# Optimization experiments

Measured on AMD Instinct MI355X. Metric: run time of the kernel, lower is better.

The kernel has to match this reference:

```python
import jax, jax.numpy as jnp
import numpy as np

B, P, D_IN, D_MOD, N_HEADS = 512, 64, 64, 256, 4

def _ln(x, g, b):
    m = x.mean(-1, keepdims=True)
    v = ((x - m) ** 2).mean(-1, keepdims=True)
    return (x - m) / jnp.sqrt(v + 1e-5) * g + b

def _lin(x, w, b):
    return x @ w.T + b

def _mha(q, k, v, in_w, in_b, out_w, out_b, n_heads):
    # Faithful to torch nn.MultiheadAttention(batch_first=False): dim0=seq, dim1=batch.
    S, N, E = q.shape
    dh = E // n_heads
    wq, wk, wv = jnp.split(in_w, 3, axis=0)
    bq, bk, bv = jnp.split(in_b, 3)
    qp = _lin(q, wq, bq).reshape(S, N, n_heads, dh)
    kp = _lin(k, wk, bk).reshape(S, N, n_heads, dh)
    vp = _lin(v, wv, bv).reshape(S, N, n_heads, dh)
    scores = jnp.einsum('snhd,tnhd->nhst', qp, kp) * (1.0 / np.sqrt(dh))
    attn = jax.nn.softmax(scores, axis=-1)
    o = jnp.einsum('nhst,tnhd->snhd', attn, vp).reshape(S, N, E)
    return _lin(o, out_w, out_b)

def _forward(x, emb_w, emb_b, emb_g, emb_beta, post_w, post_b, post_g, post_beta,
             attn_qw, attn_qb, attn_kw, attn_kb, attn_vw, attn_vb,
             attn_inw, attn_inb, attn_outw, attn_outb, attn_g, attn_beta,
             player_w, player_b, player_g, player_beta,
             team_w, team_b, team_g, team_beta,
             pre_w, pre_b, pre_g, pre_beta, lnf_g, lnf_b, pred_w, pred_b):
    # embedding: LinearWithLayerNorm = LayerNorm(Linear(x))
    p = _ln(_lin(x, emb_w, emb_b), emb_g, emb_beta)
    # post_embedding: ResidualLinearWithLayerNorm = LayerNorm(Linear(x)) + x
    p = _ln(_lin(p, post_w, post_b), post_g, post_beta) + p
    for i in range(2):
        res = p
        q = _lin(p, attn_qw[i], attn_qb[i])
        k = _lin(p, attn_kw[i], attn_kb[i])
        v = _lin(p, attn_vw[i], attn_vb[i])
        a = _mha(q, k, v, attn_inw[i], attn_inb[i], attn_outw[i], attn_outb[i], N_HEADS)
        p = _ln(a, attn_g[i], attn_beta[i]) + res
    for i in range(2):
        p = _ln(_lin(p, player_w[i], player_b[i]), player_g[i], player_beta[i]) + p
    # segment reduce: padded-ragged scatter + sum == masked sum over the player axis.
    # NOTE: original code computes BOTH masks as original[:,:,-1]==1 (bug preserved).
    mask = (x[:, :, -1] == 1).astype(p.dtype)  # [B, P]
    home = jnp.einsum('bpd,bp->bd', p, mask)
    away = home
    teams = jnp.concatenate([home, away], axis=1)  # [B, 2*d_mod]
    for i in range(2):
        teams = _ln(_lin(teams, team_w[i], team_b[i]), team_g[i], team_beta[i]) + teams
    o = _ln(_lin(teams, pre_w, pre_b), pre_g, pre_beta)
    o = _ln(o, lnf_g, lnf_b)
    o = _lin(o, pred_w, pred_b)[:, 0]  # squeeze(dim=1)
    return o


def setup_inputs() -> dict:
    key = jax.random.key(0)
    ks = iter(jax.random.split(key, 64))
    def nrm(shape):
        return jax.random.normal(next(ks), shape, jnp.float32) * 0.02
    x = jax.random.normal(next(ks), (B, P, D_IN), jnp.float32)
    flag = jax.random.bernoulli(next(ks), 0.5, (B, P)).astype(jnp.float32)
    x = x.at[:, :, -1].set(flag)  # binary home-team indicator channel
    d, d2 = D_MOD, 2 * D_MOD
    return dict(
        x=x,
        emb_w=nrm((d, D_IN)), emb_b=jnp.zeros(d), emb_g=jnp.ones(d), emb_beta=jnp.zeros(d),
        post_w=nrm((d, d)), post_b=jnp.zeros(d), post_g=jnp.ones(d), post_beta=jnp.zeros(d),
        attn_qw=nrm((2, d, d)), attn_qb=jnp.zeros((2, d)),
        attn_kw=nrm((2, d, d)), attn_kb=jnp.zeros((2, d)),
        attn_vw=nrm((2, d, d)), attn_vb=jnp.zeros((2, d)),
        attn_inw=nrm((2, 3 * d, d)), attn_inb=jnp.zeros((2, 3 * d)),
        attn_outw=nrm((2, d, d)), attn_outb=jnp.zeros((2, d)),
        attn_g=jnp.ones((2, d)), attn_beta=jnp.zeros((2, d)),
        player_w=nrm((2, d, d)), player_b=jnp.zeros((2, d)),
        player_g=jnp.ones((2, d)), player_beta=jnp.zeros((2, d)),
        team_w=nrm((2, d2, d2)), team_b=jnp.zeros((2, d2)),
        team_g=jnp.ones((2, d2)), team_beta=jnp.zeros((2, d2)),
        pre_w=nrm((d, d2)), pre_b=jnp.zeros(d), pre_g=jnp.ones(d), pre_beta=jnp.zeros(d),
        lnf_g=jnp.ones(d), lnf_b=jnp.zeros(d),
        pred_w=nrm((1, d)), pred_b=jnp.zeros(1),
    )


def reference(x, emb_w, emb_b, emb_g, emb_beta, post_w, post_b, post_g, post_beta,
              attn_qw, attn_qb, attn_kw, attn_kb, attn_vw, attn_vb,
              attn_inw, attn_inb, attn_outw, attn_outb, attn_g, attn_beta,
              player_w, player_b, player_g, player_beta,
              team_w, team_b, team_g, team_beta,
              pre_w, pre_b, pre_g, pre_beta, lnf_g, lnf_b, pred_w, pred_b):
    return _forward(x, emb_w, emb_b, emb_g, emb_beta, post_w, post_b, post_g, post_beta,
                    attn_qw, attn_qb, attn_kw, attn_kb, attn_vw, attn_vb,
                    attn_inw, attn_inb, attn_outw, attn_outb, attn_g, attn_beta,
                    player_w, player_b, player_g, player_beta,
                    team_w, team_b, team_g, team_beta,
                    pre_w, pre_b, pre_g, pre_beta, lnf_g, lnf_b, pred_w, pred_b)
```

## Files before the change

kernel.cpp:

```cpp
#include <hip/hip_runtime.h>
#include <math.h>


typedef __bf16 bf16x8 __attribute__((ext_vector_type(8)));
typedef __bf16 bf16x4 __attribute__((ext_vector_type(4)));
typedef __bf16 bf16x2 __attribute__((ext_vector_type(2)));
typedef float  f32x4  __attribute__((ext_vector_type(4)));
typedef unsigned short u16;
typedef unsigned short u16x8 __attribute__((ext_vector_type(8)));

__device__ __forceinline__ u16 f2b(float f) {
    unsigned int u = __builtin_bit_cast(unsigned int, f);
    return (u16)((u + 0x7fffu + ((u >> 16) & 1u)) >> 16);
}
__device__ __forceinline__ float b2f(u16 u) {
    unsigned int v = ((unsigned int)u) << 16;
    return __builtin_bit_cast(float, v);
}
__device__ __forceinline__ bf16x8 ld2x64(const u16* p) {
    bf16x4 lo = *(const bf16x4*)p;
    bf16x4 hi = *(const bf16x4*)(p + 4);
    return __builtin_shufflevector(lo, hi, 0, 1, 2, 3, 4, 5, 6, 7);
}
__device__ __forceinline__ bf16x8 ld4x32(const u16* p) {
    bf16x2 a = *(const bf16x2*)p,     b = *(const bf16x2*)(p + 2);
    bf16x2 c = *(const bf16x2*)(p + 4), d = *(const bf16x2*)(p + 6);
    bf16x4 lo = __builtin_shufflevector(a, b, 0, 1, 2, 3);
    bf16x4 hi = __builtin_shufflevector(c, d, 0, 1, 2, 3);
    return __builtin_shufflevector(lo, hi, 0, 1, 2, 3, 4, 5, 6, 7);
}
__device__ __forceinline__ void split8(const float* __restrict__ s,
                                       bf16x8& hi, bf16x8& lo) {
    u16x8 h, l;
    #pragma unroll
    for (int j = 0; j < 8; ++j) {
        float v  = s[j];
        u16  hb  = f2b(v);
        h[j] = hb;
        l[j] = f2b(v - b2f(hb));
    }
    hi = __builtin_bit_cast(bf16x8, h);
    lo = __builtin_bit_cast(bf16x8, l);
}

template<int IN, bool LN, bool RES, bool AF32, int OMODE>
__device__ __forceinline__
void gemm_body(const void* __restrict__ Xa, const void* __restrict__ Xb, int ldX,
               const u16* __restrict__ Whi, const u16* __restrict__ Wlo,
               const float* __restrict__ bias,
               const float* __restrict__ g, const float* __restrict__ beta,
               const u16* __restrict__ resh, const u16* __restrict__ resl,
               int ldRes, void* __restrict__ Y0, void* __restrict__ Y1, int ldY,
               u16* __restrict__ Wb)
{
    constexpr int KT = IN / 32;
    const int tid = threadIdx.x;
    const int wv = tid >> 6, lane = tid & 63;
    const int quad = lane >> 4, l16 = lane & 15;
    const long arow = (long)blockIdx.x * 64 + wv * 16 + l16;

    const u16* sbase[8];
    int sdst[8];
    #pragma unroll
    for (int i = 0; i < 8; ++i) {
        int cid = tid + i * 256;
        int plane = cid >> 10, nt = (cid >> 6) & 15, slot = cid & 63;
        int q = slot >> 4, c = slot & 15;
        sbase[i] = (plane ? Wlo : Whi) + (long)(nt * 16 + c) * IN + q * 8;
        sdst[i]  = (plane * 16 + nt) * 512 + slot * 8;
    }
    u16x8 wreg[8];
    auto issueW = [&](int kt) {
        #pragma unroll
        for (int i = 0; i < 8; ++i) wreg[i] = *(const u16x8*)(sbase[i] + kt * 32);
    };
    auto commitW = [&](int buf) {
        #pragma unroll
        for (int i = 0; i < 8; ++i)
            *(u16x8*)&Wb[buf * 16384 + sdst[i]] = wreg[i];
    };

    bf16x8 ah[3], al[3];
    auto loadA = [&](int kt) {
        int s = kt % 3;
        long aofs = arow * (long)ldX + kt * 32 + quad * 8;
        if constexpr (AF32) {
            float av[8];
            *(f32x4*)&av[0] = *(const f32x4*)&((const float*)Xa)[aofs];
            *(f32x4*)&av[4] = *(const f32x4*)&((const float*)Xa)[aofs + 4];
            split8(av, ah[s], al[s]);
        } else {
            ah[s] = *(const bf16x8*)&((const u16*)Xa)[aofs];
            al[s] = *(const bf16x8*)&((const u16*)Xb)[aofs];
        }
    };

    f32x4 acc[16];
    #pragma unroll
    for (int nt = 0; nt < 16; ++nt) acc[nt] = f32x4{0.f, 0.f, 0.f, 0.f};

    issueW(0);
    commitW(0);
    if (KT > 1) issueW(1);
    loadA(0);
    if (KT > 1) loadA(1);
    __syncthreads();

    #pragma unroll
    for (int kt = 0; kt < KT; ++kt) {
        if (kt + 2 < KT) loadA(kt + 2);
        const u16* wb = Wb + (kt & 1) * 16384;
        const int s = kt % 3;
        #pragma unroll
        for (int nt = 0; nt < 16; ++nt) {
            bf16x8 bhi = *(const bf16x8*)&wb[nt * 512 + lane * 8];
            bf16x8 blo = *(const bf16x8*)&wb[(16 + nt) * 512 + lane * 8];
            acc[nt] = __builtin_amdgcn_mfma_f32_16x16x32_bf16(al[s], bhi, acc[nt], 0, 0, 0);
            acc[nt] = __builtin_amdgcn_mfma_f32_16x16x32_bf16(ah[s], blo, acc[nt], 0, 0, 0);
            acc[nt] = __builtin_amdgcn_mfma_f32_16x16x32_bf16(ah[s], bhi, acc[nt], 0, 0, 0);
        }
        if (kt + 1 < KT) {
            commitW((kt + 1) & 1);
            if (kt + 2 < KT) issueW(kt + 2);
            __syncthreads();
        }
    }

    #pragma unroll
    for (int nt = 0; nt < 16; ++nt) {
        float bc = bias[nt * 16 + l16];
        #pragma unroll
        for (int r = 0; r < 4; ++r) acc[nt][r] += bc;
    }

    float mean[4], rstd[4];
    if constexpr (LN) {
        float s1[4] = {0, 0, 0, 0}, s2[4] = {0, 0, 0, 0};
        #pragma unroll
        for (int nt = 0; nt < 16; ++nt)
            #pragma unroll
            for (int r = 0; r < 4; ++r) {
                s1[r] += acc[nt][r];
                s2[r] += acc[nt][r] * acc[nt][r];
            }
        #pragma unroll
        for (int off = 1; off < 16; off <<= 1)
            #pragma unroll
            for (int r = 0; r < 4; ++r) {
                s1[r] += __shfl_xor(s1[r], off, 64);
                s2[r] += __shfl_xor(s2[r], off, 64);
            }
        #pragma unroll
        for (int r = 0; r < 4; ++r) {
            mean[r] = s1[r] * (1.0f / 256.f);
            float var = s2[r] * (1.0f / 256.f) - mean[r] * mean[r];
            rstd[r] = rsqrtf(var + 1e-5f);
        }
    }
    #pragma unroll
    for (int nt = 0; nt < 16; ++nt) {
        int col = nt * 16 + l16;
        float gc = 1.f, bc2 = 0.f;
        if constexpr (LN) { gc = g[col]; bc2 = beta[col]; }
        #pragma unroll
        for (int r = 0; r < 4; ++r) {
            long row = (long)blockIdx.x * 64 + wv * 16 + quad * 4 + r;
            float v = acc[nt][r];
            if constexpr (LN) v = (v - mean[r]) * rstd[r] * gc + bc2;
            if constexpr (RES)
                v += b2f(resh[row * ldRes + col]) + b2f(resl[row * ldRes + col]);
            long yofs = row * ldY + col;
            if constexpr (OMODE == 0) {
                ((float*)Y0)[yofs] = v;
            } else if constexpr (OMODE == 1) {
                u16 hb = f2b(v);
                ((u16*)Y0)[yofs] = hb;
                ((u16*)Y1)[yofs] = f2b(v - b2f(hb));
            } else {
                ((u16*)Y0)[yofs] = f2b(v);
            }
        }
    }
}

template<int IN, bool LN, bool RES, bool AF32, int OMODE>
__global__ __launch_bounds__(256)
void gemm_kernel(const void* __restrict__ Xa, const void* __restrict__ Xb, int ldX,
                 const u16* __restrict__ Whi, const u16* __restrict__ Wlo,
                 const float* __restrict__ bias,
                 const float* __restrict__ g, const float* __restrict__ beta,
                 const u16* __restrict__ resh, const u16* __restrict__ resl,
                 int ldRes, void* __restrict__ Y0, void* __restrict__ Y1, int ldY)
{
    __shared__ u16 Wb[32768];
    gemm_body<IN, LN, RES, AF32, OMODE>(Xa, Xb, ldX, Whi, Wlo, bias, g,
                                        beta, resh, resl, ldRes, Y0, Y1,
                                        ldY, Wb);
}

__global__ __launch_bounds__(256)
void qkv_proj(const u16* __restrict__ ph, const u16* __restrict__ pl,
              const u16* __restrict__ cwL, const float* __restrict__ cb,
              u16* __restrict__ qb, u16* __restrict__ kb, u16* __restrict__ vh)
{
    __shared__ u16 Wb[32768];
    int wsel = blockIdx.y;
    const u16* whi = cwL + (long)wsel * 65536;
    const u16* wlo = cwL + 393216 + (long)wsel * 65536;
    u16* Y = (wsel == 0) ? qb : (wsel == 1) ? kb : vh;
    gemm_body<256, false, false, false, 2>(
        ph, pl, 256, whi, wlo, cb + wsel * 256, nullptr, nullptr,
        nullptr, nullptr, 0, Y, nullptr, 256, Wb);
}

__global__ __launch_bounds__(256)
void combine_kernel(const float* __restrict__ inw, const float* __restrict__ inb,
                    const float* __restrict__ qw, const float* __restrict__ kw,
                    const float* __restrict__ vw, const float* __restrict__ qb,
                    const float* __restrict__ kb, const float* __restrict__ vb,
                    u16* __restrict__ cw, float* __restrict__ cb)
{
    int idx = blockIdx.y, L = idx / 3, wsel = idx % 3;
    const float* Wa = inw + (long)L * 768 * 256 + wsel * 65536;
    const float* ba = inb + L * 768 + wsel * 256;
    const float* Wf = (wsel == 0 ? qw : wsel == 1 ? kw : vw) + (long)L * 65536;
    const float* bf = (wsel == 0 ? qb : wsel == 1 ? kb : vb) + L * 256;

    int o = blockIdx.x, j = threadIdx.x;
    float s = 0.f;
    for (int mm = 0; mm < 256; ++mm)
        s += Wa[o * 256 + mm] * Wf[mm * 256 + j];
    u16 hb = f2b(s);
    cw[(long)idx * 65536 + o * 256 + j] = hb;
    cw[393216 + (long)idx * 65536 + o * 256 + j] = f2b(s - b2f(hb));

    __shared__ float red[256];
    red[j] = Wa[o * 256 + j] * bf[j];
    __syncthreads();
    for (int st = 128; st > 0; st >>= 1) {
        if (j < st) red[j] += red[j + st];
        __syncthreads();
    }
    if (j == 0) cb[idx * 256 + o] = red[0] + ba[o];
}

__global__ __launch_bounds__(256)
void cast_split_multi(const float* s0, u16* d0, int n0,
                      const float* s1, u16* d1, int n1,
                      const float* s2, u16* d2, int n2,
                      const float* s3, u16* d3, int n3,
                      const float* s4, u16* d4, int n4,
                      const float* s5, u16* d5, int n5)
{
    const float* s; u16* d; int n;
    switch (blockIdx.y) {
        case 0: s = s0; d = d0; n = n0; break;
        case 1: s = s1; d = d1; n = n1; break;
        case 2: s = s2; d = d2; n = n2; break;
        case 3: s = s3; d = d3; n = n3; break;
        case 4: s = s4; d = d4; n = n4; break;
        default: s = s5; d = d5; n = n5; break;
    }
    int i = (blockIdx.x * 256 + threadIdx.x) * 4;
    if (i >= n) return;
    float4 v = *(const float4*)&s[i];
    ushort4 h, l;
    h.x = f2b(v.x); l.x = f2b(v.x - b2f(h.x));
    h.y = f2b(v.y); l.y = f2b(v.y - b2f(h.y));
    h.z = f2b(v.z); l.z = f2b(v.z - b2f(h.z));
    h.w = f2b(v.w); l.w = f2b(v.w - b2f(h.w));
    *(ushort4*)&d[i] = h;
    *(ushort4*)&d[n + i] = l;
}

#define VTS 66
#define PS  68
#define EXP2SCALE 0.18033688089184986f

__global__ __launch_bounds__(256)
void attn_kernel(const u16* __restrict__ qbuf, const u16* __restrict__ kbuf,
                 const u16* __restrict__ vh,
                 u16* __restrict__ ofh, u16* __restrict__ ofl)
{
    const int n = blockIdx.x, h = blockIdx.y, sq = blockIdx.z;
    const int tid = threadIdx.x;
    const int wv = tid >> 6, lane = tid & 63;
    const int quad = lane >> 4, l16 = lane & 15;

    __shared__ u16 Vth[64 * VTS];
    __shared__ u16 Pbh[4][32 * PS];

    bf16x8 qf[2][2];
    #pragma unroll
    for (int rt = 0; rt < 2; ++rt)
        #pragma unroll
        for (int kc = 0; kc < 2; ++kc) {
            long s = sq * 128 + wv * 32 + rt * 16 + l16;
            qf[rt][kc] = *(const bf16x8*)&qbuf[(s * 64 + n) * 256 + h * 64
                                               + kc * 32 + quad * 8];
        }

    f32x4 o[2][4];
    #pragma unroll
    for (int rt = 0; rt < 2; ++rt)
        #pragma unroll
        for (int dt = 0; dt < 4; ++dt) o[rt][dt] = f32x4{0.f, 0.f, 0.f, 0.f};
    float l_run[2][4] = {{0.f, 0.f, 0.f, 0.f}, {0.f, 0.f, 0.f, 0.f}};

    for (int tb = 0; tb < 8; ++tb) {
        __syncthreads();
        for (int i = tid; i < 512; i += 256) {
            int t = i >> 3, c = i & 7;
            u16x8 hvv = *(const u16x8*)&vh[((long)(tb * 64 + t) * 64 + n) * 256
                                           + h * 64 + c * 8];
            #pragma unroll
            for (int j = 0; j < 8; ++j)
                Vth[(c * 8 + j) * VTS + t] = hvv[j];
        }
        __syncthreads();

        f32x4 sA[2][4];
        #pragma unroll
        for (int rt = 0; rt < 2; ++rt)
            #pragma unroll
            for (int tt = 0; tt < 4; ++tt) sA[rt][tt] = f32x4{0.f, 0.f, 0.f, 0.f};
        #pragma unroll
        for (int kc = 0; kc < 2; ++kc)
            #pragma unroll
            for (int tt = 0; tt < 4; ++tt) {
                bf16x8 kf = *(const bf16x8*)
                    &kbuf[((long)(tb * 64 + tt * 16 + l16) * 64 + n) * 256
                          + h * 64 + kc * 32 + quad * 8];
                sA[0][tt] = __builtin_amdgcn_mfma_f32_16x16x32_bf16(
                    qf[0][kc], kf, sA[0][tt], 0, 0, 0);
                sA[1][tt] = __builtin_amdgcn_mfma_f32_16x16x32_bf16(
                    qf[1][kc], kf, sA[1][tt], 0, 0, 0);
            }

        #pragma unroll
        for (int rt = 0; rt < 2; ++rt)
            #pragma unroll
            for (int r = 0; r < 4; ++r) {
                float p0 = exp2f(sA[rt][0][r] * EXP2SCALE);
                float p1 = exp2f(sA[rt][1][r] * EXP2SCALE);
                float p2 = exp2f(sA[rt][2][r] * EXP2SCALE);
                float p3 = exp2f(sA[rt][3][r] * EXP2SCALE);
                int prow = (rt * 16 + quad * 4 + r) * PS + l16;
                Pbh[wv][prow +  0] = f2b(p0);
                Pbh[wv][prow + 16] = f2b(p1);
                Pbh[wv][prow + 32] = f2b(p2);
                Pbh[wv][prow + 48] = f2b(p3);
                l_run[rt][r] += (p0 + p1) + (p2 + p3);
            }

        #pragma unroll
        for (int kc = 0; kc < 2; ++kc) {
            bf16x8 pfh[2];
            #pragma unroll
            for (int rt = 0; rt < 2; ++rt)
                pfh[rt] = ld2x64(&Pbh[wv][(rt * 16 + l16) * PS
                                          + kc * 32 + quad * 8]);
            #pragma unroll
            for (int dt = 0; dt < 4; ++dt) {
                bf16x8 vfh = ld4x32(&Vth[(dt * 16 + l16) * VTS
                                         + kc * 32 + quad * 8]);
                o[0][dt] = __builtin_amdgcn_mfma_f32_16x16x32_bf16(
                    pfh[0], vfh, o[0][dt], 0, 0, 0);
                o[1][dt] = __builtin_amdgcn_mfma_f32_16x16x32_bf16(
                    pfh[1], vfh, o[1][dt], 0, 0, 0);
            }
        }
    }

    #pragma unroll
    for (int off = 1; off < 16; off <<= 1)
        #pragma unroll
        for (int rt = 0; rt < 2; ++rt)
            #pragma unroll
            for (int r = 0; r < 4; ++r)
                l_run[rt][r] += __shfl_xor(l_run[rt][r], off, 64);

    #pragma unroll
    for (int rt = 0; rt < 2; ++rt)
        #pragma unroll
        for (int r = 0; r < 4; ++r) {
            float inv = 1.0f / l_run[rt][r];
            long s = sq * 128 + wv * 32 + rt * 16 + quad * 4 + r;
            #pragma unroll
            for (int dt = 0; dt < 4; ++dt) {
                long idx = (s * 64 + n) * 256 + h * 64 + dt * 16 + l16;
                float val = o[rt][dt][r] * inv;
                u16 hb = f2b(val);
                ofh[idx] = hb;
                ofl[idx] = f2b(val - b2f(hb));
            }
        }
}

__global__ __launch_bounds__(256)
void team_reduce_kernel(const float* __restrict__ x, const u16* __restrict__ ph,
                        const u16* __restrict__ pl, float* __restrict__ teams)
{
    int b = blockIdx.x, d = threadIdx.x;
    float acc = 0.f;
    for (int pp = 0; pp < 64; ++pp) {
        float flag = x[((long)b * 64 + pp) * 64 + 63];
        if (flag == 1.0f) {
            long idx = ((long)b * 64 + pp) * 256 + d;
            acc += b2f(ph[idx]) + b2f(pl[idx]);
        }
    }
    teams[(long)b * 512 + d]       = acc;
    teams[(long)b * 512 + 256 + d] = acc;
}

template<int IN, int OUT, bool RES>
__global__ __launch_bounds__(256)
void tail_gemm(const float* __restrict__ X,
               const u16* __restrict__ Whi, const u16* __restrict__ Wlo,
               const float* __restrict__ bias,
               const float* __restrict__ g, const float* __restrict__ beta,
               const float* __restrict__ res, float* __restrict__ Y)
{
    constexpr int NTW = OUT / 64;
    constexpr int KT  = IN / 32;
    const int tid = threadIdx.x;
    const int wv = tid >> 6, lane = tid & 63;
    const int quad = lane >> 4, l16 = lane & 15;
    const int row0 = blockIdx.x * 16;
    const int colbase = wv * (OUT / 4);

    f32x4 acc[NTW];
    #pragma unroll
    for (int nt = 0; nt < NTW; ++nt) acc[nt] = f32x4{0.f, 0.f, 0.f, 0.f};

    #pragma unroll
    for (int kt = 0; kt < KT; ++kt) {
        float av[8];
        long aofs = (long)(row0 + l16) * IN + kt * 32 + quad * 8;
        *(f32x4*)&av[0] = *(const f32x4*)&X[aofs];
        *(f32x4*)&av[4] = *(const f32x4*)&X[aofs + 4];
        bf16x8 ah, al;
        split8(av, ah, al);
        #pragma unroll
        for (int nt = 0; nt < NTW; ++nt) {
            long wofs = (long)(colbase + nt * 16 + l16) * IN + kt * 32 + quad * 8;
            bf16x8 bhi = *(const bf16x8*)&Whi[wofs];
            bf16x8 blo = *(const bf16x8*)&Wlo[wofs];
            acc[nt] = __builtin_amdgcn_mfma_f32_16x16x32_bf16(al, bhi, acc[nt], 0, 0, 0);
            acc[nt] = __builtin_amdgcn_mfma_f32_16x16x32_bf16(ah, blo, acc[nt], 0, 0, 0);
            acc[nt] = __builtin_amdgcn_mfma_f32_16x16x32_bf16(ah, bhi, acc[nt], 0, 0, 0);
        }
    }

    #pragma unroll
    for (int nt = 0; nt < NTW; ++nt) {
        float bc = bias[colbase + nt * 16 + l16];
        #pragma unroll
        for (int r = 0; r < 4; ++r) acc[nt][r] += bc;
    }

    float s1[4] = {0, 0, 0, 0}, s2[4] = {0, 0, 0, 0};
    #pragma unroll
    for (int nt = 0; nt < NTW; ++nt)
        #pragma unroll
        for (int r = 0; r < 4; ++r) {
            s1[r] += acc[nt][r];
            s2[r] += acc[nt][r] * acc[nt][r];
        }
    #pragma unroll
    for (int off = 1; off < 16; off <<= 1)
        #pragma unroll
        for (int r = 0; r < 4; ++r) {
            s1[r] += __shfl_xor(s1[r], off, 64);
            s2[r] += __shfl_xor(s2[r], off, 64);
        }
    __shared__ float r1[64], r2[64];
    if (l16 == 0) {
        #pragma unroll
        for (int r = 0; r < 4; ++r) {
            r1[wv * 16 + quad * 4 + r] = s1[r];
            r2[wv * 16 + quad * 4 + r] = s2[r];
        }
    }
    __syncthreads();
    float mean[4], rstd[4];
    #pragma unroll
    for (int r = 0; r < 4; ++r) {
        int rr = quad * 4 + r;
        float t1 = r1[rr] + r1[16 + rr] + r1[32 + rr] + r1[48 + rr];
        float t2 = r2[rr] + r2[16 + rr] + r2[32 + rr] + r2[48 + rr];
        mean[r] = t1 * (1.0f / OUT);
        float var = t2 * (1.0f / OUT) - mean[r] * mean[r];
        rstd[r] = rsqrtf(var + 1e-5f);
    }
    #pragma unroll
    for (int nt = 0; nt < NTW; ++nt) {
        int col = colbase + nt * 16 + l16;
        float gc = g[col], bc2 = beta[col];
        #pragma unroll
        for (int r = 0; r < 4; ++r) {
            int row = row0 + quad * 4 + r;
            float v = (acc[nt][r] - mean[r]) * rstd[r] * gc + bc2;
            if constexpr (RES) v += res[(long)row * OUT + col];
            Y[(long)row * OUT + col] = v;
        }
    }
}

__global__ __launch_bounds__(64)
void ln_kernel(const float* __restrict__ X, const float* __restrict__ g,
               const float* __restrict__ b, float* __restrict__ Y)
{
    int row = blockIdx.x, lane = threadIdx.x;
    float4 v = *(const float4*)&X[(long)row * 256 + lane * 4];
    float s1 = v.x + v.y + v.z + v.w;
    float s2 = v.x*v.x + v.y*v.y + v.z*v.z + v.w*v.w;
    #pragma unroll
    for (int off = 32; off > 0; off >>= 1) {
        s1 += __shfl_xor(s1, off, 64);
        s2 += __shfl_xor(s2, off, 64);
    }
    float mean = s1 * (1.f / 256.f);
    float rstd = rsqrtf(s2 * (1.f / 256.f) - mean * mean + 1e-5f);
    float4 gg = *(const float4*)&g[lane * 4];
    float4 bb = *(const float4*)&b[lane * 4];
    float4 o;
    o.x = (v.x - mean) * rstd * gg.x + bb.x;
    o.y = (v.y - mean) * rstd * gg.y + bb.y;
    o.z = (v.z - mean) * rstd * gg.z + bb.z;
    o.w = (v.w - mean) * rstd * gg.w + bb.w;
    *(float4*)&Y[(long)row * 256 + lane * 4] = o;
}

__global__ __launch_bounds__(64)
void pred_kernel(const float* __restrict__ X, const float* __restrict__ pw,
                 const float* __restrict__ pb, float* __restrict__ out)
{
    int row = blockIdx.x, lane = threadIdx.x;
    float4 v = *(const float4*)&X[(long)row * 256 + lane * 4];
    float4 w = *(const float4*)&pw[lane * 4];
    float s = v.x*w.x + v.y*w.y + v.z*w.z + v.w*w.w;
    #pragma unroll
    for (int off = 32; off > 0; off >>= 1) s += __shfl_xor(s, off, 64);
    if (lane == 0) out[row] = s + pb[0];
}

extern "C" void kernel_launch(void* const* d_in, const int* in_sizes, int n_in,
                              void* d_out, int out_size, void* d_ws, size_t ws_size,
                              hipStream_t stream)
{
    const float* x         = (const float*)d_in[0];
    const float* emb_w     = (const float*)d_in[1];
    const float* emb_b     = (const float*)d_in[2];
    const float* emb_g     = (const float*)d_in[3];
    const float* emb_beta  = (const float*)d_in[4];
    const float* post_w    = (const float*)d_in[5];
    const float* post_b    = (const float*)d_in[6];
    const float* post_g    = (const float*)d_in[7];
    const float* post_beta = (const float*)d_in[8];
    const float* attn_qw   = (const float*)d_in[9];
    const float* attn_qb   = (const float*)d_in[10];
    const float* attn_kw   = (const float*)d_in[11];
    const float* attn_kb   = (const float*)d_in[12];
    const float* attn_vw   = (const float*)d_in[13];
    const float* attn_vb   = (const float*)d_in[14];
    const float* attn_inw  = (const float*)d_in[15];
    const float* attn_inb  = (const float*)d_in[16];
    const float* attn_outw = (const float*)d_in[17];
    const float* attn_outb = (const float*)d_in[18];
    const float* attn_g    = (const float*)d_in[19];
    const float* attn_beta = (const float*)d_in[20];
    const float* player_w  = (const float*)d_in[21];
    const float* player_b  = (const float*)d_in[22];
    const float* player_g  = (const float*)d_in[23];
    const float* player_bt = (const float*)d_in[24];
    const float* team_w    = (const float*)d_in[25];
    const float* team_b    = (const float*)d_in[26];
    const float* team_g    = (const float*)d_in[27];
    const float* team_beta = (const float*)d_in[28];
    const float* pre_w     = (const float*)d_in[29];
    const float* pre_b     = (const float*)d_in[30];
    const float* pre_g     = (const float*)d_in[31];
    const float* pre_beta  = (const float*)d_in[32];
    const float* lnf_g     = (const float*)d_in[33];
    const float* lnf_b     = (const float*)d_in[34];
    const float* pred_w    = (const float*)d_in[35];
    const float* pred_b    = (const float*)d_in[36];

    char* base = (char*)d_ws;
    const size_t NR = (size_t)32768 * 256;
    u16* ph  = (u16*)base;  base += NR * 2;
    u16* pl  = (u16*)base;  base += NR * 2;
    u16* ofh = (u16*)base;  base += NR * 2;
    u16* ofl = (u16*)base;  base += NR * 2;
    u16* vh  = (u16*)base;  base += NR * 2;
    u16* qb  = (u16*)base;  base += NR * 2;
    u16* kb  = (u16*)base;  base += NR * 2;
    float* teams0 = (float*)base; base += (size_t)512 * 512 * 4;
    float* teams1 = (float*)base; base += (size_t)512 * 512 * 4;
    float* o5     = (float*)base; base += (size_t)512 * 256 * 4;
    u16* emb_wp    = (u16*)base;  base += (size_t)2 * 16384 * 2;
    u16* post_wp   = (u16*)base;  base += (size_t)2 * 65536 * 2;
    u16* outw_p    = (u16*)base;  base += (size_t)2 * 131072 * 2;
    u16* player_wp = (u16*)base;  base += (size_t)2 * 131072 * 2;
    u16* team_wp   = (u16*)base;  base += (size_t)2 * 524288 * 2;
    u16* pre_wp    = (u16*)base;  base += (size_t)2 * 131072 * 2;
    u16* cwb       = (u16*)base;  base += (size_t)2 * 393216 * 2;
    float* cbf     = (float*)base; base += (size_t)1536 * 4;

    cast_split_multi<<<dim3(512, 6), 256, 0, stream>>>(
        emb_w, emb_wp, 16384,
        post_w, post_wp, 65536,
        attn_outw, outw_p, 131072,
        player_w, player_wp, 131072,
        team_w, team_wp, 524288,
        pre_w, pre_wp, 131072);

    combine_kernel<<<dim3(256, 6), 256, 0, stream>>>(
        attn_inw, attn_inb, attn_qw, attn_kw, attn_vw,
        attn_qb, attn_kb, attn_vb, cwb, cbf);

    gemm_kernel<64, true, false, true, 1><<<512, 256, 0, stream>>>(
        x, nullptr, 64, emb_wp, emb_wp + 16384, emb_b, emb_g, emb_beta,
        nullptr, nullptr, 0, ph, pl, 256);
    gemm_kernel<256, true, true, false, 1><<<512, 256, 0, stream>>>(
        ph, pl, 256, post_wp, post_wp + 65536, post_b, post_g, post_beta,
        ph, pl, 256, ph, pl, 256);

    for (int L = 0; L < 2; ++L) {
        qkv_proj<<<dim3(512, 3), 256, 0, stream>>>(
            ph, pl, cwb + (size_t)L * 3 * 65536, cbf + L * 768, qb, kb, vh);
        attn_kernel<<<dim3(64, 4, 4), 256, 0, stream>>>(qb, kb, vh, ofh, ofl);
        gemm_kernel<256, true, true, false, 1><<<512, 256, 0, stream>>>(
            ofh, ofl, 256, outw_p + (size_t)L * 65536,
            outw_p + 131072 + (size_t)L * 65536, attn_outb + L * 256,
            attn_g + L * 256, attn_beta + L * 256, ph, pl, 256, ph, pl, 256);
    }

    for (int L = 0; L < 2; ++L)
        gemm_kernel<256, true, true, false, 1><<<512, 256, 0, stream>>>(
            ph, pl, 256, player_wp + (size_t)L * 65536,
            player_wp + 131072 + (size_t)L * 65536, player_b + L * 256,
            player_g + L * 256, player_bt + L * 256, ph, pl, 256, ph, pl, 256);

    team_reduce_kernel<<<512, 256, 0, stream>>>(x, ph, pl, teams0);

    tail_gemm<512, 512, true><<<32, 256, 0, stream>>>(
        teams0, team_wp, team_wp + 524288, team_b,
        team_g, team_beta, teams0, teams1);
    tail_gemm<512, 512, true><<<32, 256, 0, stream>>>(
        teams1, team_wp + 262144, team_wp + 524288 + 262144, team_b + 512,
        team_g + 512, team_beta + 512, teams1, teams0);

    tail_gemm<512, 256, false><<<32, 256, 0, stream>>>(
        teams0, pre_wp, pre_wp + 131072, pre_b, pre_g, pre_beta,
        nullptr, o5);
    ln_kernel<<<512, 64, 0, stream>>>(o5, lnf_g, lnf_b, o5);
    pred_kernel<<<512, 64, 0, stream>>>(o5, pred_w, pred_b, (float*)d_out);
}
```

Baseline: 773.0 us.

## Split GEMM columns across waves and stage weights via global_load_lds

```diff
diff --git a/kernel.cpp b/kernel.cpp
--- a/kernel.cpp
+++ b/kernel.cpp
@@ -8,6 +8,10 @@
 typedef float  f32x4  __attribute__((ext_vector_type(4)));
 typedef unsigned short u16;
 typedef unsigned short u16x8 __attribute__((ext_vector_type(8)));
+
+typedef __attribute__((address_space(1))) const unsigned char gas_char;
+typedef __attribute__((address_space(3))) unsigned char las_char;
+#define GLL16(g, l) __builtin_amdgcn_global_load_lds((gas_char*)(g), (las_char*)(l), 16, 0, 0)
 
 __device__ __forceinline__ u16 f2b(float f) {
     unsigned int u = __builtin_bit_cast(unsigned int, f);
@@ -57,51 +61,52 @@
     const int tid = threadIdx.x;
     const int wv = tid >> 6, lane = tid & 63;
     const int quad = lane >> 4, l16 = lane & 15;
-    const long arow = (long)blockIdx.x * 64 + wv * 16 + l16;
+    const long rowblk = (long)blockIdx.x * 64;
+    const int colbase = wv * 64;
+
+    __shared__ float r1[4][64], r2[4][64];
 
     const u16* sbase[8];
-    int sdst[8];
     #pragma unroll
     for (int i = 0; i < 8; ++i) {
         int cid = tid + i * 256;
         int plane = cid >> 10, nt = (cid >> 6) & 15, slot = cid & 63;
         int q = slot >> 4, c = slot & 15;
         sbase[i] = (plane ? Wlo : Whi) + (long)(nt * 16 + c) * IN + q * 8;
-        sdst[i]  = (plane * 16 + nt) * 512 + slot * 8;
-    }
-    u16x8 wreg[8];
-    auto issueW = [&](int kt) {
-        #pragma unroll
-        for (int i = 0; i < 8; ++i) wreg[i] = *(const u16x8*)(sbase[i] + kt * 32);
+    }
+    auto stageW = [&](int kt, int buf) {
+        #pragma unroll
+        for (int i = 0; i < 8; ++i)
+            GLL16(sbase[i] + kt * 32,
+                  (unsigned char*)Wb + buf * 32768 + (tid + i * 256) * 16);
     };
-    auto commitW = [&](int buf) {
-        #pragma unroll
-        for (int i = 0; i < 8; ++i)
-            *(u16x8*)&Wb[buf * 16384 + sdst[i]] = wreg[i];
-    };
-
-    bf16x8 ah[3], al[3];
+
+    bf16x8 ah[3][4], al[3][4];
     auto loadA = [&](int kt) {
         int s = kt % 3;
-        long aofs = arow * (long)ldX + kt * 32 + quad * 8;
-        if constexpr (AF32) {
-            float av[8];
-            *(f32x4*)&av[0] = *(const f32x4*)&((const float*)Xa)[aofs];
-            *(f32x4*)&av[4] = *(const f32x4*)&((const float*)Xa)[aofs + 4];
-            split8(av, ah[s], al[s]);
-        } else {
-            ah[s] = *(const bf16x8*)&((const u16*)Xa)[aofs];
-            al[s] = *(const bf16x8*)&((const u16*)Xb)[aofs];
+        #pragma unroll
+        for (int rt = 0; rt < 4; ++rt) {
+            long aofs = (rowblk + rt * 16 + l16) * (long)ldX + kt * 32 + quad * 8;
+            if constexpr (AF32) {
+                float av[8];
+                *(f32x4*)&av[0] = *(const f32x4*)&((const float*)Xa)[aofs];
+                *(f32x4*)&av[4] = *(const f32x4*)&((const float*)Xa)[aofs + 4];
+                split8(av, ah[s][rt], al[s][rt]);
+            } else {
+                ah[s][rt] = *(const bf16x8*)&((const u16*)Xa)[aofs];
+                al[s][rt] = *(const bf16x8*)&((const u16*)Xb)[aofs];
+            }
         }
     };
 
-    f32x4 acc[16];
-    #pragma unroll
-    for (int nt = 0; nt < 16; ++nt) acc[nt] = f32x4{0.f, 0.f, 0.f, 0.f};
-
-    issueW(0);
-    commitW(0);
-    if (KT > 1) issueW(1);
+    f32x4 acc[4][4];
+    #pragma unroll
+    for (int nt = 0; nt < 4; ++nt)
+        #pragma unroll
+        for (int rt = 0; rt < 4; ++rt) acc[nt][rt] = f32x4{0.f, 0.f, 0.f, 0.f};
+
+    stageW(0, 0);
+    if (KT > 1) stageW(1, 1);
     loadA(0);
     if (KT > 1) loadA(1);
     __syncthreads();
@@ -112,74 +117,106 @@
         const u16* wb = Wb + (kt & 1) * 16384;
         const int s = kt % 3;
         #pragma unroll
-        for (int nt = 0; nt < 16; ++nt) {
-            bf16x8 bhi = *(const bf16x8*)&wb[nt * 512 + lane * 8];
-            bf16x8 blo = *(const bf16x8*)&wb[(16 + nt) * 512 + lane * 8];
-            acc[nt] = __builtin_amdgcn_mfma_f32_16x16x32_bf16(al[s], bhi, acc[nt], 0, 0, 0);
-            acc[nt] = __builtin_amdgcn_mfma_f32_16x16x32_bf16(ah[s], blo, acc[nt], 0, 0, 0);
-            acc[nt] = __builtin_amdgcn_mfma_f32_16x16x32_bf16(ah[s], bhi, acc[nt], 0, 0, 0);
+        for (int nt = 0; nt < 4; ++nt) {
+            const int ntg = wv * 4 + nt;
+            bf16x8 bhi = *(const bf16x8*)&wb[ntg * 512 + lane * 8];
+            bf16x8 blo = *(const bf16x8*)&wb[(16 + ntg) * 512 + lane * 8];
+            #pragma unroll
+            for (int rt = 0; rt < 4; ++rt) {
+                acc[nt][rt] = __builtin_amdgcn_mfma_f32_16x16x32_bf16(al[s][rt], bhi, acc[nt][rt], 0, 0, 0);
+                acc[nt][rt] = __builtin_amdgcn_mfma_f32_16x16x32_bf16(ah[s][rt], blo, acc[nt][rt], 0, 0, 0);
+                acc[nt][rt] = __builtin_amdgcn_mfma_f32_16x16x32_bf16(ah[s][rt], bhi, acc[nt][rt], 0, 0, 0);
+            }
         }
         if (kt + 1 < KT) {
-            commitW((kt + 1) & 1);
-            if (kt + 2 < KT) issueW(kt + 2);
             __syncthreads();
-        }
-    }
-
-    #pragma unroll
-    for (int nt = 0; nt < 16; ++nt) {
-        float bc = bias[nt * 16 + l16];
-        #pragma unroll
-        for (int r = 0; r < 4; ++r) acc[nt][r] += bc;
-    }
-
-    float mean[4], rstd[4];
+            if (kt + 2 < KT) stageW(kt + 2, kt & 1);
+        }
+    }
+
+    #pragma unroll
+    for (int nt = 0; nt < 4; ++nt) {
+        float bc = bias[colbase + nt * 16 + l16];
+        #pragma unroll
+        for (int rt = 0; rt < 4; ++rt)
+            #pragma unroll
+            for (int r = 0; r < 4; ++r) acc[nt][rt][r] += bc;
+    }
+
+    float mean[4][4], rstd[4][4];
     if constexpr (LN) {
-        float s1[4] = {0, 0, 0, 0}, s2[4] = {0, 0, 0, 0};
-        #pragma unroll
-        for (int nt = 0; nt < 16; ++nt)
+        float s1[4][4], s2[4][4];
+        #pragma unroll
+        for (int rt = 0; rt < 4; ++rt)
+            #pragma unroll
+            for (int r = 0; r < 4; ++r) { s1[rt][r] = 0.f; s2[rt][r] = 0.f; }
+        #pragma unroll
+        for (int nt = 0; nt < 4; ++nt)
+            #pragma unroll
+            for (int rt = 0; rt < 4; ++rt)
+                #pragma unroll
+                for (int r = 0; r < 4; ++r) {
+                    s1[rt][r] += acc[nt][rt][r];
+                    s2[rt][r] += acc[nt][rt][r] * acc[nt][rt][r];
+                }
+        #pragma unroll
+        for (int off = 1; off < 16; off <<= 1)
+            #pragma unroll
+            for (int rt = 0; rt < 4; ++rt)
+                #pragma unroll
+                for (int r = 0; r < 4; ++r) {
+                    s1[rt][r] += __shfl_xor(s1[rt][r], off, 64);
+                    s2[rt][r] += __shfl_xor(s2[rt][r], off, 64);
+                }
+        __syncthreads();
+        if (l16 == 0) {
+            #pragma unroll
+            for (int rt = 0; rt < 4; ++rt)
+                #pragma unroll
+                for (int r = 0; r < 4; ++r) {
+                    r1[wv][rt * 16 + quad * 4 + r] = s1[rt][r];
+                    r2[wv][rt * 16 + quad * 4 + r] = s2[rt][r];
+                }
+        }
+        __syncthreads();
+        #pragma unroll
+        for (int rt = 0; rt < 4; ++rt)
             #pragma unroll
             for (int r = 0; r < 4; ++r) {
-                s1[r] += acc[nt][r];
-                s2[r] += acc[nt][r] * acc[nt][r];
-            }
-        #pragma unroll
-        for (int off = 1; off < 16; off <<= 1)
-            #pragma unroll
-            for (int r = 0; r < 4; ++r) {
-                s1[r] += __shfl_xor(s1[r], off, 64);
-                s2[r] += __shfl_xor(s2[r], off, 64);
-            }
-        #pragma unroll
-        for (int r = 0; r < 4; ++r) {
-            mean[r] = s1[r] * (1.0f / 256.f);
-            float var = s2[r] * (1.0f / 256.f) - mean[r] * mean[r];
-            rstd[r] = rsqrtf(var + 1e-5f);
-        }
-    }
-    #pragma unroll
-    for (int nt = 0; nt < 16; ++nt) {
-        int col = nt * 16 + l16;
+                int row = rt * 16 + quad * 4 + r;
+                float t1 = r1[0][row] + r1[1][row] + r1[2][row] + r1[3][row];
+                float t2 = r2[0][row] + r2[1][row] + r2[2][row] + r2[3][row];
+                mean[rt][r] = t1 * (1.0f / 256.f);
+                float var = t2 * (1.0f / 256.f) - mean[rt][r] * mean[rt][r];
+                rstd[rt][r] = rsqrtf(var + 1e-5f);
+            }
+    }
+
+    #pragma unroll
+    for (int nt = 0; nt < 4; ++nt) {
+        int col = colbase + nt * 16 + l16;
         float gc = 1.f, bc2 = 0.f;
         if constexpr (LN) { gc = g[col]; bc2 = beta[col]; }
         #pragma unroll
-        for (int r = 0; r < 4; ++r) {
-            long row = (long)blockIdx.x * 64 + wv * 16 + quad * 4 + r;
-            float v = acc[nt][r];
-            if constexpr (LN) v = (v - mean[r]) * rstd[r] * gc + bc2;
-            if constexpr (RES)
-                v += b2f(resh[row * ldRes + col]) + b2f(resl[row * ldRes + col]);
-            long yofs = row * ldY + col;
-            if constexpr (OMODE == 0) {
-                ((float*)Y0)[yofs] = v;
-            } else if constexpr (OMODE == 1) {
-                u16 hb = f2b(v);
-                ((u16*)Y0)[yofs] = hb;
-                ((u16*)Y1)[yofs] = f2b(v - b2f(hb));
-            } else {
-                ((u16*)Y0)[yofs] = f2b(v);
-            }
-        }
+        for (int rt = 0; rt < 4; ++rt)
+            #pragma unroll
+            for (int r = 0; r < 4; ++r) {
+                long row = rowblk + rt * 16 + quad * 4 + r;
+                float v = acc[nt][rt][r];
+                if constexpr (LN) v = (v - mean[rt][r]) * rstd[rt][r] * gc + bc2;
+                if constexpr (RES)
+                    v += b2f(resh[row * ldRes + col]) + b2f(resl[row * ldRes + col]);
+                long yofs = row * ldY + col;
+                if constexpr (OMODE == 0) {
+                    ((float*)Y0)[yofs] = v;
+                } else if constexpr (OMODE == 1) {
+                    u16 hb = f2b(v);
+                    ((u16*)Y0)[yofs] = hb;
+                    ((u16*)Y1)[yofs] = f2b(v - b2f(hb));
+                } else {
+                    ((u16*)Y0)[yofs] = f2b(v);
+                }
+            }
     }
 }
 
```

New measurement: 903.5 us. 16.9% more time.

## Fuse team reduction into last player GEMM and fuse tail LN/pred

Applied to the files above, without the earlier changes.

```diff
diff --git a/kernel.cpp b/kernel.cpp
--- a/kernel.cpp
+++ b/kernel.cpp
@@ -43,7 +43,7 @@
     lo = __builtin_bit_cast(bf16x8, l);
 }
 
-template<int IN, bool LN, bool RES, bool AF32, int OMODE>
+template<int IN, bool LN, bool RES, bool AF32, int OMODE, bool TEAM>
 __device__ __forceinline__
 void gemm_body(const void* __restrict__ Xa, const void* __restrict__ Xb, int ldX,
                const u16* __restrict__ Whi, const u16* __restrict__ Wlo,
@@ -51,6 +51,7 @@
                const float* __restrict__ g, const float* __restrict__ beta,
                const u16* __restrict__ resh, const u16* __restrict__ resl,
                int ldRes, void* __restrict__ Y0, void* __restrict__ Y1, int ldY,
+               const float* __restrict__ xmask, float* __restrict__ teams,
                u16* __restrict__ Wb)
 {
     constexpr int KT = IN / 32;
@@ -157,6 +158,50 @@
             rstd[r] = rsqrtf(var + 1e-5f);
         }
     }
+
+    if constexpr (TEAM) {
+        float m[4];
+        #pragma unroll
+        for (int r = 0; r < 4; ++r) {
+            long row = (long)blockIdx.x * 64 + wv * 16 + quad * 4 + r;
+            m[r] = (xmask[row * 64 + 63] == 1.0f) ? 1.0f : 0.0f;
+        }
+        float ts[16];
+        #pragma unroll
+        for (int nt = 0; nt < 16; ++nt) {
+            int col = nt * 16 + l16;
+            float gc = g[col], bc2 = beta[col];
+            ts[nt] = 0.f;
+            #pragma unroll
+            for (int r = 0; r < 4; ++r) {
+                long row = (long)blockIdx.x * 64 + wv * 16 + quad * 4 + r;
+                float v = (acc[nt][r] - mean[r]) * rstd[r] * gc + bc2;
+                v += b2f(resh[row * ldRes + col]) + b2f(resl[row * ldRes + col]);
+                ts[nt] += m[r] * v;
+            }
+        }
+        #pragma unroll
+        for (int nt = 0; nt < 16; ++nt) {
+            ts[nt] += __shfl_xor(ts[nt], 16, 64);
+            ts[nt] += __shfl_xor(ts[nt], 32, 64);
+        }
+        __syncthreads();
+        float* tsum = (float*)Wb;
+        if (quad == 0) {
+            #pragma unroll
+            for (int nt = 0; nt < 16; ++nt)
+                tsum[wv * 256 + nt * 16 + l16] = ts[nt];
+        }
+        __syncthreads();
+        if (tid < 256) {
+            float tot = tsum[tid] + tsum[256 + tid]
+                      + tsum[512 + tid] + tsum[768 + tid];
+            teams[(long)blockIdx.x * 512 + tid]       = tot;
+            teams[(long)blockIdx.x * 512 + 256 + tid] = tot;
+        }
+        return;
+    }
+
     #pragma unroll
     for (int nt = 0; nt < 16; ++nt) {
         int col = nt * 16 + l16;
@@ -183,19 +228,20 @@
     }
 }
 
-template<int IN, bool LN, bool RES, bool AF32, int OMODE>
+template<int IN, bool LN, bool RES, bool AF32, int OMODE, bool TEAM>
 __global__ __launch_bounds__(256)
 void gemm_kernel(const void* __restrict__ Xa, const void* __restrict__ Xb, int ldX,
                  const u16* __restrict__ Whi, const u16* __restrict__ Wlo,
                  const float* __restrict__ bias,
                  const float* __restrict__ g, const float* __restrict__ beta,
                  const u16* __restrict__ resh, const u16* __restrict__ resl,
-                 int ldRes, void* __restrict__ Y0, void* __restrict__ Y1, int ldY)
+                 int ldRes, void* __restrict__ Y0, void* __restrict__ Y1, int ldY,
+                 const float* __restrict__ xmask, float* __restrict__ teams)
 {
     __shared__ u16 Wb[32768];
-    gemm_body<IN, LN, RES, AF32, OMODE>(Xa, Xb, ldX, Whi, Wlo, bias, g,
-                                        beta, resh, resl, ldRes, Y0, Y1,
-                                        ldY, Wb);
+    gemm_body<IN, LN, RES, AF32, OMODE, TEAM>(Xa, Xb, ldX, Whi, Wlo, bias, g,
+                                              beta, resh, resl, ldRes, Y0, Y1,
+                                              ldY, xmask, teams, Wb);
 }
 
 __global__ __launch_bounds__(256)
@@ -208,9 +254,9 @@
     const u16* whi = cwL + (long)wsel * 65536;
     const u16* wlo = cwL + 393216 + (long)wsel * 65536;
     u16* Y = (wsel == 0) ? qb : (wsel == 1) ? kb : vh;
-    gemm_body<256, false, false, false, 2>(
+    gemm_body<256, false, false, false, 2, false>(
         ph, pl, 256, whi, wlo, cb + wsel * 256, nullptr, nullptr,
-        nullptr, nullptr, 0, Y, nullptr, 256, Wb);
+        nullptr, nullptr, 0, Y, nullptr, 256, nullptr, nullptr, Wb);
 }
 
 __global__ __launch_bounds__(256)
@@ -397,23 +443,6 @@
         }
 }
 
-__global__ __launch_bounds__(256)
-void team_reduce_kernel(const float* __restrict__ x, const u16* __restrict__ ph,
-                        const u16* __restrict__ pl, float* __restrict__ teams)
-{
-    int b = blockIdx.x, d = threadIdx.x;
-    float acc = 0.f;
-    for (int pp = 0; pp < 64; ++pp) {
-        float flag = x[((long)b * 64 + pp) * 64 + 63];
-        if (flag == 1.0f) {
-            long idx = ((long)b * 64 + pp) * 256 + d;
-            acc += b2f(ph[idx]) + b2f(pl[idx]);
-        }
-    }
-    teams[(long)b * 512 + d]       = acc;
-    teams[(long)b * 512 + 256 + d] = acc;
-}
-
 template<int IN, int OUT, bool RES>
 __global__ __launch_bounds__(256)
 void tail_gemm(const float* __restrict__ X,
@@ -508,42 +537,146 @@
     }
 }
 
-__global__ __launch_bounds__(64)
-void ln_kernel(const float* __restrict__ X, const float* __restrict__ g,
-               const float* __restrict__ b, float* __restrict__ Y)
-{
-    int row = blockIdx.x, lane = threadIdx.x;
-    float4 v = *(const float4*)&X[(long)row * 256 + lane * 4];
-    float s1 = v.x + v.y + v.z + v.w;
-    float s2 = v.x*v.x + v.y*v.y + v.z*v.z + v.w*v.w;
-    #pragma unroll
-    for (int off = 32; off > 0; off >>= 1) {
-        s1 += __shfl_xor(s1, off, 64);
-        s2 += __shfl_xor(s2, off, 64);
-    }
-    float mean = s1 * (1.f / 256.f);
-    float rstd = rsqrtf(s2 * (1.f / 256.f) - mean * mean + 1e-5f);
-    float4 gg = *(const float4*)&g[lane * 4];
-    float4 bb = *(const float4*)&b[lane * 4];
-    float4 o;
-    o.x = (v.x - mean) * rstd * gg.x + bb.x;
-    o.y = (v.y - mean) * rstd * gg.y + bb.y;
-    o.z = (v.z - mean) * rstd * gg.z + bb.z;
-    o.w = (v.w - mean) * rstd * gg.w + bb.w;
-    *(float4*)&Y[(long)row * 256 + lane * 4] = o;
-}
-
-__global__ __launch_bounds__(64)
-void pred_kernel(const float* __restrict__ X, const float* __restrict__ pw,
-                 const float* __restrict__ pb, float* __restrict__ out)
-{
-    int row = blockIdx.x, lane = threadIdx.x;
-    float4 v = *(const float4*)&X[(long)row * 256 + lane * 4];
-    float4 w = *(const float4*)&pw[lane * 4];
-    float s = v.x*w.x + v.y*w.y + v.z*w.z + v.w*w.w;
-    #pragma unroll
-    for (int off = 32; off > 0; off >>= 1) s += __shfl_xor(s, off, 64);
-    if (lane == 0) out[row] = s + pb[0];
+__global__ __launch_bounds__(256)
+void tail_pred(const float* __restrict__ X,
+               const u16* __restrict__ Whi, const u16* __restrict__ Wlo,
+               const float* __restrict__ bias,
+               const float* __restrict__ g, const float* __restrict__ beta,
+               const float* __restrict__ lnf_g, const float* __restrict__ lnf_b,
+               const float* __restrict__ pw, const float* __restrict__ pb,
+               float* __restrict__ out)
+{
+    constexpr int IN = 512, OUT = 256, NTW = 4, KT = 16;
+    const int tid = threadIdx.x;
+    const int wv = tid >> 6, lane = tid & 63;
+    const int quad = lane >> 4, l16 = lane & 15;
+    const int row0 = blockIdx.x * 16;
+    const int colbase = wv * 64;
+
+    f32x4 acc[NTW];
+    #pragma unroll
+    for (int nt = 0; nt < NTW; ++nt) acc[nt] = f32x4{0.f, 0.f, 0.f, 0.f};
+
+    #pragma unroll
+    for (int kt = 0; kt < KT; ++kt) {
+        float av[8];
+        long aofs = (long)(row0 + l16) * IN + kt * 32 + quad * 8;
+        *(f32x4*)&av[0] = *(const f32x4*)&X[aofs];
+        *(f32x4*)&av[4] = *(const f32x4*)&X[aofs + 4];
+        bf16x8 ah, al;
+        split8(av, ah, al);
+        #pragma unroll
+        for (int nt = 0; nt < NTW; ++nt) {
+            long wofs = (long)(colbase + nt * 16 + l16) * IN + kt * 32 + quad * 8;
+            bf16x8 bhi = *(const bf16x8*)&Whi[wofs];
+            bf16x8 blo = *(const bf16x8*)&Wlo[wofs];
+            acc[nt] = __builtin_amdgcn_mfma_f32_16x16x32_bf16(al, bhi, acc[nt], 0, 0, 0);
+            acc[nt] = __builtin_amdgcn_mfma_f32_16x16x32_bf16(ah, blo, acc[nt], 0, 0, 0);
+            acc[nt] = __builtin_amdgcn_mfma_f32_16x16x32_bf16(ah, bhi, acc[nt], 0, 0, 0);
+        }
+    }
+    #pragma unroll
+    for (int nt = 0; nt < NTW; ++nt) {
+        float bc = bias[colbase + nt * 16 + l16];
+        #pragma unroll
+        for (int r = 0; r < 4; ++r) acc[nt][r] += bc;
+    }
+
+    __shared__ float r1[64], r2[64];
+    float s1[4] = {0, 0, 0, 0}, s2[4] = {0, 0, 0, 0};
+    #pragma unroll
+    for (int nt = 0; nt < NTW; ++nt)
+        #pragma unroll
+        for (int r = 0; r < 4; ++r) {
+            s1[r] += acc[nt][r];
+            s2[r] += acc[nt][r] * acc[nt][r];
+        }
+    #pragma unroll
+    for (int off = 1; off < 16; off <<= 1)
+        #pragma unroll
+        for (int r = 0; r < 4; ++r) {
+            s1[r] += __shfl_xor(s1[r], off, 64);
+            s2[r] += __shfl_xor(s2[r], off, 64);
+        }
+    if (l16 == 0)
+        #pragma unroll
+        for (int r = 0; r < 4; ++r) {
+            r1[wv * 16 + quad * 4 + r] = s1[r];
+            r2[wv * 16 + quad * 4 + r] = s2[r];
+        }
+    __syncthreads();
+    float vv[NTW][4];
+    #pragma unroll
+    for (int r = 0; r < 4; ++r) {
+        int rr = quad * 4 + r;
+        float t1 = r1[rr] + r1[16 + rr] + r1[32 + rr] + r1[48 + rr];
+        float t2 = r2[rr] + r2[16 + rr] + r2[32 + rr] + r2[48 + rr];
+        float mean = t1 * (1.0f / OUT);
+        float rstd = rsqrtf(t2 * (1.0f / OUT) - mean * mean + 1e-5f);
+        #pragma unroll
+        for (int nt = 0; nt < NTW; ++nt) {
+            int col = colbase + nt * 16 + l16;
+            vv[nt][r] = (acc[nt][r] - mean) * rstd * g[col] + beta[col];
+        }
+    }
+    float u1[4] = {0, 0, 0, 0}, u2[4] = {0, 0, 0, 0};
+    #pragma unroll
+    for (int nt = 0; nt < NTW; ++nt)
+        #pragma unroll
+        for (int r = 0; r < 4; ++r) {
+            u1[r] += vv[nt][r];
+            u2[r] += vv[nt][r] * vv[nt][r];
+        }
+    #pragma unroll
+    for (int off = 1; off < 16; off <<= 1)
+        #pragma unroll
+        for (int r = 0; r < 4; ++r) {
+            u1[r] += __shfl_xor(u1[r], off, 64);
+            u2[r] += __shfl_xor(u2[r], off, 64);
+        }
+    __syncthreads();
+    if (l16 == 0)
+        #pragma unroll
+        for (int r = 0; r < 4; ++r) {
+            r1[wv * 16 + quad * 4 + r] = u1[r];
+            r2[wv * 16 + quad * 4 + r] = u2[r];
+        }
+    __syncthreads();
+    float pd[4];
+    #pragma unroll
+    for (int r = 0; r < 4; ++r) {
+        int rr = quad * 4 + r;
+        float t1 = r1[rr] + r1[16 + rr] + r1[32 + rr] + r1[48 + rr];
+        float t2 = r2[rr] + r2[16 + rr] + r2[32 + rr] + r2[48 + rr];
+        float mean = t1 * (1.0f / OUT);
+        float rstd = rsqrtf(t2 * (1.0f / OUT) - mean * mean + 1e-5f);
+        pd[r] = 0.f;
+        #pragma unroll
+        for (int nt = 0; nt < NTW; ++nt) {
+            int col = colbase + nt * 16 + l16;
+            float v2 = (vv[nt][r] - mean) * rstd * lnf_g[col] + lnf_b[col];
+            pd[r] += v2 * pw[col];
+        }
+    }
+    #pragma unroll
+    for (int off = 1; off < 16; off <<= 1)
+        #pragma unroll
+        for (int r = 0; r < 4; ++r)
+            pd[r] += __shfl_xor(pd[r], off, 64);
+    __syncthreads();
+    if (l16 == 0)
+        #pragma unroll
+        for (int r = 0; r < 4; ++r)
+            r1[wv * 16 + quad * 4 + r] = pd[r];
+    __syncthreads();
+    if (wv == 0 && l16 == 0) {
+        #pragma unroll
+        for (int r = 0; r < 4; ++r) {
+            int rr = quad * 4 + r;
+            out[row0 + rr] = r1[rr] + r1[16 + rr] + r1[32 + rr] + r1[48 + rr]
+                           + pb[0];
+        }
+    }
 }
 
 extern "C" void kernel_launch(void* const* d_in, const int* in_sizes, int n_in,
@@ -599,7 +732,6 @@
     u16* kb  = (u16*)base;  base += NR * 2;
     float* teams0 = (float*)base; base += (size_t)512 * 512 * 4;
     float* teams1 = (float*)base; base += (size_t)512 * 512 * 4;
-    float* o5     = (float*)base; base += (size_t)512 * 256 * 4;
     u16* emb_wp    = (u16*)base;  base += (size_t)2 * 16384 * 2;
     u16* post_wp   = (u16*)base;  base += (size_t)2 * 65536 * 2;
     u16* outw_p    = (u16*)base;  base += (size_t)2 * 131072 * 2;
@@ -621,30 +753,31 @@
         attn_inw, attn_inb, attn_qw, attn_kw, attn_vw,
         attn_qb, attn_kb, attn_vb, cwb, cbf);
 
-    gemm_kernel<64, true, false, true, 1><<<512, 256, 0, stream>>>(
+    gemm_kernel<64, true, false, true, 1, false><<<512, 256, 0, stream>>>(
         x, nullptr, 64, emb_wp, emb_wp + 16384, emb_b, emb_g, emb_beta,
-        nullptr, nullptr, 0, ph, pl, 256);
-    gemm_kernel<256, true, true, false, 1><<<512, 256, 0, stream>>>(
+        nullptr, nullptr, 0, ph, pl, 256, nullptr, nullptr);
+    gemm_kernel<256, true, true, false, 1, false><<<512, 256, 0, stream>>>(
         ph, pl, 256, post_wp, post_wp + 65536, post_b, post_g, post_beta,
-        ph, pl, 256, ph, pl, 256);
+        ph, pl, 256, ph, pl, 256, nullptr, nullptr);
 
     for (int L = 0; L < 2; ++L) {
         qkv_proj<<<dim3(512, 3), 256, 0, stream>>>(
             ph, pl, cwb + (size_t)L * 3 * 65536, cbf + L * 768, qb, kb, vh);
         attn_kernel<<<dim3(64, 4, 4), 256, 0, stream>>>(qb, kb, vh, ofh, ofl);
-        gemm_kernel<256, true, true, false, 1><<<512, 256, 0, stream>>>(
+        gemm_kernel<256, true, true, false, 1, false><<<512, 256, 0, stream>>>(
             ofh, ofl, 256, outw_p + (size_t)L * 65536,
             outw_p + 131072 + (size_t)L * 65536, attn_outb + L * 256,
-            attn_g + L * 256, attn_beta + L * 256, ph, pl, 256, ph, pl, 256);
-    }
-
-    for (int L = 0; L < 2; ++L)
-        gemm_kernel<256, true, true, false, 1><<<512, 256, 0, stream>>>(
-            ph, pl, 256, player_wp + (size_t)L * 65536,
-            player_wp + 131072 + (size_t)L * 65536, player_b + L * 256,
-            player_g + L * 256, player_bt + L * 256, ph, pl, 256, ph, pl, 256);
-
-    team_reduce_kernel<<<512, 256, 0, stream>>>(x, ph, pl, teams0);
+            attn_g + L * 256, attn_beta + L * 256, ph, pl, 256, ph, pl, 256,
+            nullptr, nullptr);
+    }
+
+    gemm_kernel<256, true, true, false, 1, false><<<512, 256, 0, stream>>>(
+        ph, pl, 256, player_wp, player_wp + 131072, player_b,
+        player_g, player_bt, ph, pl, 256, ph, pl, 256, nullptr, nullptr);
+    gemm_kernel<256, true, true, false, 1, true><<<512, 256, 0, stream>>>(
+        ph, pl, 256, player_wp + 65536, player_wp + 131072 + 65536,
+        player_b + 256, player_g + 256, player_bt + 256, ph, pl, 256,
+        nullptr, nullptr, 256, x, teams0);
 
     tail_gemm<512, 512, true><<<32, 256, 0, stream>>>(
         teams0, team_wp, team_wp + 524288, team_b,
@@ -653,9 +786,7 @@
         teams1, team_wp + 262144, team_wp + 524288 + 262144, team_b + 512,
         team_g + 512, team_beta + 512, teams1, teams0);
 
-    tail_gemm<512, 256, false><<<32, 256, 0, stream>>>(
+    tail_pred<<<32, 256, 0, stream>>>(
         teams0, pre_wp, pre_wp + 131072, pre_b, pre_g, pre_beta,
-        nullptr, o5);
-    ln_kernel<<<512, 64, 0, stream>>>(o5, lnf_g, lnf_b, o5);
-    pred_kernel<<<512, 64, 0, stream>>>(o5, pred_w, pred_b, (float*)d_out);
-}
+        lnf_g, lnf_b, pred_w, pred_b, (float*)d_out);
+}
```

New measurement: 750.1 us. -3.0%, faster.
